# Optimization experiments

Measured on AMD Instinct MI355X. Metric: run time of the kernel, lower is better.

Reference implementation:

```python
import jax, jax.numpy as jnp
import numpy as np

SIGMA = 1.0
S = 1.0 / (2.0 * SIGMA * SIGMA)  # 0.5


def setup_inputs() -> dict:
    key = jax.random.key(0)
    k1, k2 = jax.random.split(key)
    inputs = jax.random.normal(k1, (32, 4096, 3), dtype=jnp.float32)  # (B, N, D) point cloud
    # stars initialized RandomUniform(-1, 1) in the original build()
    stars = jax.random.uniform(k2, (1024, 3), minval=-1.0, maxval=1.0, dtype=jnp.float32)  # (M, D)
    return {"inputs": inputs, "stars": stars}


def reference(inputs, stars):
    # out[b, m] = sum_n exp(-S * ||inputs[b, n] - stars[m]||^2)
    # Use ||a-b||^2 = ||a||^2 - 2 a.b + ||b||^2 to avoid the (B, M, N, D) diff tensor.
    x2 = jnp.sum(inputs * inputs, axis=-1)          # (B, N)
    s2 = jnp.sum(stars * stars, axis=-1)            # (M,)
    cross = jnp.einsum('bnd,md->bmn', inputs, stars)  # (B, M, N)
    d2 = x2[:, None, :] - 2.0 * cross + s2[None, :, None]  # (B, M, N)
    return jnp.sum(jnp.exp(-S * d2), axis=2)        # (B, M)
```

## Files before the change

### kernel.cpp

```cpp
#include <hip/hip_runtime.h>


#define NB 32
#define NN 4096
#define NM 1024
#define NCHUNK 32
#define NPB (NN / NCHUNK)
#define TPB 128
#define MPT (NM / TPB)

__device__ __forceinline__ float exp2_hw(float x) {
#if __has_builtin(__builtin_amdgcn_exp2f)
    return __builtin_amdgcn_exp2f(x);
#else
    float r;
    asm("v_exp_f32 %0, %1" : "=v"(r) : "v"(x));
    return r;
#endif
}

__global__ __launch_bounds__(256) void gau_zero(float* __restrict__ out) {
    out[blockIdx.x * 256 + threadIdx.x] = 0.0f;
}

__global__ __launch_bounds__(TPB) void gau_main(const float* __restrict__ inputs,
                                                const float* __restrict__ stars,
                                                float* __restrict__ out) {
    constexpr float C2  = 0.72134752044448169f;
    constexpr float L2E = 1.44269504088896340f;

    const int b     = blockIdx.x / NCHUNK;
    const int chunk = blockIdx.x % NCHUNK;
    const int t     = threadIdx.x;

    __shared__ float4 pts[NPB];

    {
        const float* p = inputs + ((size_t)b * NN + (size_t)chunk * NPB + t) * 3;
        float x = p[0], y = p[1], z = p[2];
        float q = -C2 * x * x - C2 * y * y - C2 * z * z;
        pts[t] = make_float4(x, y, z, exp2_hw(q));
    }

    float Sx[MPT], Sy[MPT], Sz[MPT], K[MPT];
#pragma unroll
    for (int k = 0; k < MPT; ++k) {
        int m = t + k * TPB;
        float sx = stars[3 * m + 0];
        float sy = stars[3 * m + 1];
        float sz = stars[3 * m + 2];
        Sx[k] = L2E * sx;
        Sy[k] = L2E * sy;
        Sz[k] = L2E * sz;
        K[k]  = -C2 * (sx * sx + sy * sy + sz * sz);
    }

    float acc[MPT];
#pragma unroll
    for (int k = 0; k < MPT; ++k) acc[k] = 0.0f;

    __syncthreads();

#pragma unroll 4
    for (int i = 0; i < NPB; ++i) {
        float4 p = pts[i];
#pragma unroll
        for (int k = 0; k < MPT; ++k) {
            float inner = fmaf(Sx[k], p.x, fmaf(Sy[k], p.y, fmaf(Sz[k], p.z, K[k])));
            float e = exp2_hw(inner);
            acc[k] = fmaf(p.w, e, acc[k]);
        }
    }

    float* ob = out + (size_t)b * NM;
#pragma unroll
    for (int k = 0; k < MPT; ++k) {
        atomicAdd(ob + t + k * TPB, acc[k]);
    }
}

extern "C" void kernel_launch(void* const* d_in, const int* in_sizes, int n_in,
                              void* d_out, int out_size, void* d_ws, size_t ws_size,
                              hipStream_t stream) {
    const float* inputs = (const float*)d_in[0];
    const float* stars  = (const float*)d_in[1];
    float* out = (float*)d_out;

    gau_zero<<<(NB * NM) / 256, 256, 0, stream>>>(out);
    gau_main<<<NB * NCHUNK, TPB, 0, stream>>>(inputs, stars, out);
}
```

Before: 32.95 us.

## Use packed FP32 FMA on point pairs and double threads per block

Processes two points at once with v_pk_fma_f32 through inline asm, halving the FMA instruction count in the inner loop, and stores points in shared memory as paired XY/ZE float4s. Block size goes from 128 to 256 threads, so each thread handles 4 stars instead of 8, and occupancy is hinted at 4 blocks. The exp2 transcendental count per pair is unchanged, so if v_exp_f32 dominates the gain may be small. Inline asm may also block compiler scheduling.

After: 28.30 us. 1.16x faster.

```diff
diff --git a/kernel.cpp b/kernel.cpp
--- a/kernel.cpp
+++ b/kernel.cpp
@@ -1,12 +1,15 @@
 #include <hip/hip_runtime.h>
 
+
+typedef float f32x2 __attribute__((ext_vector_type(2)));
 
 #define NB 32
 #define NN 4096
 #define NM 1024
 #define NCHUNK 32
 #define NPB (NN / NCHUNK)
-#define TPB 128
+#define NPAIR (NPB / 2)
+#define TPB 256
 #define MPT (NM / TPB)
 
 __device__ __forceinline__ float exp2_hw(float x) {
@@ -19,13 +22,19 @@
 #endif
 }
 
+__device__ __forceinline__ f32x2 pk_fma(f32x2 a, f32x2 b, f32x2 c) {
+    f32x2 d;
+    asm("v_pk_fma_f32 %0, %1, %2, %3" : "=v"(d) : "v"(a), "v"(b), "v"(c));
+    return d;
+}
+
 __global__ __launch_bounds__(256) void gau_zero(float* __restrict__ out) {
     out[blockIdx.x * 256 + threadIdx.x] = 0.0f;
 }
 
-__global__ __launch_bounds__(TPB) void gau_main(const float* __restrict__ inputs,
-                                                const float* __restrict__ stars,
-                                                float* __restrict__ out) {
+__global__ __launch_bounds__(TPB, 4) void gau_main(const float* __restrict__ inputs,
+                                                   const float* __restrict__ stars,
+                                                   float* __restrict__ out) {
     constexpr float C2  = 0.72134752044448169f;
     constexpr float L2E = 1.44269504088896340f;
 
@@ -33,49 +42,57 @@
     const int chunk = blockIdx.x % NCHUNK;
     const int t     = threadIdx.x;
 
-    __shared__ float4 pts[NPB];
+    __shared__ float4 XY[NPAIR];
+    __shared__ float4 ZE[NPAIR];
 
-    {
-        const float* p = inputs + ((size_t)b * NN + (size_t)chunk * NPB + t) * 3;
-        float x = p[0], y = p[1], z = p[2];
-        float q = -C2 * x * x - C2 * y * y - C2 * z * z;
-        pts[t] = make_float4(x, y, z, exp2_hw(q));
+    if (t < NPAIR) {
+        const float* p = inputs + ((size_t)b * NN + (size_t)chunk * NPB + 2 * (size_t)t) * 3;
+        float x0 = p[0], y0 = p[1], z0 = p[2];
+        float x1 = p[3], y1 = p[4], z1 = p[5];
+        float q0 = -C2 * x0 * x0 - C2 * y0 * y0 - C2 * z0 * z0;
+        float q1 = -C2 * x1 * x1 - C2 * y1 * y1 - C2 * z1 * z1;
+        XY[t] = make_float4(x0, x1, y0, y1);
+        ZE[t] = make_float4(z0, z1, exp2_hw(q0), exp2_hw(q1));
     }
 
-    float Sx[MPT], Sy[MPT], Sz[MPT], K[MPT];
+    f32x2 Sx2[MPT], Sy2[MPT], Sz2[MPT], K2[MPT], acc[MPT];
 #pragma unroll
     for (int k = 0; k < MPT; ++k) {
         int m = t + k * TPB;
         float sx = stars[3 * m + 0];
         float sy = stars[3 * m + 1];
         float sz = stars[3 * m + 2];
-        Sx[k] = L2E * sx;
-        Sy[k] = L2E * sy;
-        Sz[k] = L2E * sz;
-        K[k]  = -C2 * (sx * sx + sy * sy + sz * sz);
+        float a = L2E * sx, c = L2E * sy, e = L2E * sz;
+        float kk = -C2 * (sx * sx + sy * sy + sz * sz);
+        Sx2[k] = f32x2{a, a};
+        Sy2[k] = f32x2{c, c};
+        Sz2[k] = f32x2{e, e};
+        K2[k]  = f32x2{kk, kk};
+        acc[k] = f32x2{0.0f, 0.0f};
     }
-
-    float acc[MPT];
-#pragma unroll
-    for (int k = 0; k < MPT; ++k) acc[k] = 0.0f;
 
     __syncthreads();
 
-#pragma unroll 4
-    for (int i = 0; i < NPB; ++i) {
-        float4 p = pts[i];
+#pragma unroll 2
+    for (int i = 0; i < NPAIR; ++i) {
+        float4 xy = XY[i];
+        float4 ze = ZE[i];
+        f32x2 x2 = f32x2{xy.x, xy.y};
+        f32x2 y2 = f32x2{xy.z, xy.w};
+        f32x2 z2 = f32x2{ze.x, ze.y};
+        f32x2 E2 = f32x2{ze.z, ze.w};
 #pragma unroll
         for (int k = 0; k < MPT; ++k) {
-            float inner = fmaf(Sx[k], p.x, fmaf(Sy[k], p.y, fmaf(Sz[k], p.z, K[k])));
-            float e = exp2_hw(inner);
-            acc[k] = fmaf(p.w, e, acc[k]);
+            f32x2 inner = pk_fma(Sx2[k], x2, pk_fma(Sy2[k], y2, pk_fma(Sz2[k], z2, K2[k])));
+            f32x2 e2 = f32x2{exp2_hw(inner.x), exp2_hw(inner.y)};
+            acc[k] = pk_fma(E2, e2, acc[k]);
         }
     }
 
     float* ob = out + (size_t)b * NM;
 #pragma unroll
     for (int k = 0; k < MPT; ++k) {
-        atomicAdd(ob + t + k * TPB, acc[k]);
+        atomicAdd(ob + t + k * TPB, acc[k].x + acc[k].y);
     }
 }
 
```
